# Performance work log

Measured on AMD Instinct MI355X. Metric: run time of the kernel, lower is better.

Reference implementation:

```python
import jax, jax.numpy as jnp
import numpy as np

D_MODEL = 512; D_STATE = 64; D_CONV = 4; EXPAND = 1; HEADDIM = 128; NGROUPS = 2; CHUNK = 256
D_INNER = EXPAND * (D_MODEL // 2)          # 256
NHEADS = D_INNER // HEADDIM                 # 2
CONV_DIM = D_INNER + 2 * NGROUPS * D_STATE  # 512
D_IN_PROJ = CONV_DIM + NHEADS               # 514

def silu(x):
    return x * jax.nn.sigmoid(x)

def conv1x1(x, w, b):
    # x: (b,c,h,w), w: (o,c)
    return jnp.einsum('bchw,oc->bohw', x, w) + b[None, :, None, None]

def dwconv3x3(x, w, b):
    # depthwise 3x3, SAME padding; w: (c,1,3,3)
    c = x.shape[1]
    y = jax.lax.conv_general_dilated(x, w, (1, 1), 'SAME', feature_group_count=c,
                                     dimension_numbers=('NCHW', 'OIHW', 'NCHW'))
    return y + b[None, :, None, None]

def causal_dwconv1d(x, w, b):
    # x: (b,L,c); w: (c,k). Torch pads k-1 both sides then slices [:L] -> causal left pad.
    k = w.shape[1]
    xp = jnp.pad(x, ((0, 0), (k - 1, 0), (0, 0))).transpose(0, 2, 1)  # (b,c,L+k-1)
    y = jax.lax.conv_general_dilated(xp, w[:, None, :], (1,), 'VALID',
                                     feature_group_count=w.shape[0],
                                     dimension_numbers=('NCH', 'OIH', 'NCH'))
    return y.transpose(0, 2, 1) + b

def axis_attn(x, qw, qb, fw, fb, axis):
    # DualAxisAggAttn single-axis step
    qkv = conv1x1(x, qw, qb)
    c = x.shape[1]
    q, k, v = qkv[:, :1], qkv[:, 1:1 + c], qkv[:, 1 + c:]
    dim = -1 if axis == 'W' else -2
    scores = jax.nn.softmax(q, axis=dim)
    ctx = jnp.sum(k * scores, axis=dim, keepdims=True)
    out = x + jax.nn.sigmoid(v) * ctx
    return conv1x1(out, fw, fb)

def segsum(x):
    # x: (...,T) -> (...,T,T) lower-triangular segment sums, -inf above diagonal
    T = x.shape[-1]
    cs = jnp.cumsum(x, -1)
    d = cs[..., :, None] - cs[..., None, :]
    mask = jnp.tril(jnp.ones((T, T), bool))
    return jnp.where(mask, d, -jnp.inf)

def ssd(X, A, B, C, chunk):
    # Mamba2 SSD chunked scan. X: (b,l,h,p) = x*dt; A: (b,l,h) = dt*A_head; B,C: (b,l,h,n)
    b, l, h, p = X.shape; n = B.shape[-1]; c = l // chunk
    X = X.reshape(b, c, chunk, h, p)
    B = B.reshape(b, c, chunk, h, n)
    C = C.reshape(b, c, chunk, h, n)
    A = A.reshape(b, c, chunk, h).transpose(0, 3, 1, 2)  # (b,h,c,L)
    Acs = jnp.cumsum(A, -1)
    L = jnp.exp(segsum(A))  # (b,h,c,L,L) intra-chunk decay
    Yd = jnp.einsum('bclhn,bcshn,bhcls,bcshp->bclhp', C, B, L, X)
    dec = jnp.exp(Acs[..., -1:] - Acs)
    st = jnp.einsum('bclhn,bhcl,bclhp->bchpn', B, dec, X)  # chunk end-states
    st = jnp.concatenate([jnp.zeros_like(st[:, :1]), st], 1)
    dchunk = jnp.exp(segsum(jnp.pad(Acs[..., -1], ((0, 0), (0, 0), (1, 0)))))
    st = jnp.einsum('bhzc,bchpn->bzhpn', dchunk, st)[:, :-1]  # states entering each chunk
    Yo = jnp.einsum('bclhn,bchpn,bhcl->bclhp', C, st, jnp.exp(Acs))
    return (Yd + Yo).reshape(b, l, h, p)

def setup_inputs() -> dict:
    key = jax.random.key(0)
    ks = jax.random.split(key, 12)
    s = 0.02
    p = {}
    p['u'] = jax.random.normal(ks[0], (8, D_MODEL, 64, 64), jnp.float32)
    p['sc_w1'] = jax.random.normal(ks[1], (D_MODEL, D_MODEL)) * s
    p['sc_b1'] = jnp.zeros((D_MODEL,))
    p['sc_wdw'] = jax.random.normal(ks[2], (D_MODEL, 1, 3, 3)) * s
    p['sc_bdw'] = jnp.zeros((D_MODEL,))
    p['sc_w2'] = jax.random.normal(ks[3], (D_INNER, D_MODEL)) * s
    p['sc_b2'] = jnp.zeros((D_INNER,))
    p['mc_w'] = jax.random.normal(ks[4], (D_INNER, D_MODEL)) * s
    p['mc_b'] = jnp.zeros((D_INNER,))
    p['qkvW_w'] = jax.random.normal(ks[5], (1 + 2 * D_INNER, D_INNER)) * s
    p['qkvW_b'] = jnp.zeros((1 + 2 * D_INNER,))
    p['qkvH_w'] = jax.random.normal(ks[6], (1 + 2 * D_INNER, D_INNER)) * s
    p['qkvH_b'] = jnp.zeros((1 + 2 * D_INNER,))
    p['fuseW_w'] = jax.random.normal(ks[7], (D_INNER, D_INNER)) * s
    p['fuseW_b'] = jnp.zeros((D_INNER,))
    p['fuseH_w'] = jax.random.normal(ks[8], (D_INNER, D_INNER)) * s
    p['fuseH_b'] = jnp.zeros((D_INNER,))
    p['in_proj_w'] = jax.random.normal(ks[9], (D_IN_PROJ, D_INNER)) * s
    p['conv1d_w'] = jax.random.normal(ks[10], (CONV_DIM, D_CONV)) * s
    p['conv1d_b'] = jnp.zeros((CONV_DIM,))
    dt = np.exp(np.linspace(np.log(1e-3), np.log(0.1), NHEADS))
    p['dt_bias'] = jnp.asarray(dt + np.log(-np.expm1(-dt)), jnp.float32)
    p['A_log'] = jnp.asarray(np.log(np.linspace(1.0, 16.0, NHEADS)), jnp.float32)
    p['D'] = jnp.ones((NHEADS,))
    p['norm_w'] = jnp.ones((D_INNER,))
    p['outp_w'] = jax.random.normal(ks[11], (D_MODEL, 2 * D_INNER)) * s
    p['outp_b'] = jnp.zeros((D_MODEL,))
    return p

def reference(u, sc_w1, sc_b1, sc_wdw, sc_bdw, sc_w2, sc_b2, mc_w, mc_b,
              qkvW_w, qkvW_b, qkvH_w, qkvH_b, fuseW_w, fuseW_b, fuseH_w, fuseH_b,
              in_proj_w, conv1d_w, conv1d_b, dt_bias, A_log, D, norm_w, outp_w, outp_b):
    b, _, H, W = u.shape
    # short_conv branch (light_ConvBlock: 1x1 -> dw3x3 -> 1x1, all SiLU; BN folded into bias)
    z = silu(conv1x1(u, sc_w1, sc_b1))
    z = silu(dwconv3x3(z, sc_wdw, sc_bdw))
    z = silu(conv1x1(z, sc_w2, sc_b2))
    # main branch
    x = silu(conv1x1(u, mc_w, mc_b))
    x = axis_attn(x, qkvW_w, qkvW_b, fuseW_w, fuseW_b, 'W')
    x = axis_attn(x, qkvH_w, qkvH_b, fuseH_w, fuseH_b, 'H')
    seqlen = H * W
    u2 = x.transpose(0, 2, 3, 1).reshape(b, seqlen, D_INNER)  # b (h w) c
    xbcdt = u2 @ in_proj_w.T  # (b,l,d_in_proj)
    xBC = xbcdt[..., :CONV_DIM]
    dt = jax.nn.softplus(xbcdt[..., CONV_DIM:] + dt_bias)  # (b,l,h)
    A = -jnp.exp(A_log)  # (h,)
    xBC = silu(causal_dwconv1d(xBC, conv1d_w, conv1d_b))
    xs = xBC[..., :D_INNER]
    Bs = xBC[..., D_INNER:D_INNER + NGROUPS * D_STATE].reshape(b, seqlen, NGROUPS, D_STATE)
    Cs = xBC[..., D_INNER + NGROUPS * D_STATE:].reshape(b, seqlen, NGROUPS, D_STATE)
    Xh = xs.reshape(b, seqlen, NHEADS, HEADDIM)
    rep = NHEADS // NGROUPS
    Bh = jnp.repeat(Bs, rep, axis=2)
    Ch = jnp.repeat(Cs, rep, axis=2)
    y = ssd(Xh * dt[..., None], dt * A[None, None, :], Bh, Ch, CHUNK)
    y = y + Xh * D[None, None, :, None]  # D skip connection
    y = y.reshape(b, seqlen, D_INNER)
    # RMSNormGated with z=None -> plain RMSNorm
    y = y * jax.lax.rsqrt(jnp.mean(y * y, -1, keepdims=True) + 1e-5) * norm_w
    y = y.reshape(b, H, W, D_INNER).transpose(0, 3, 1, 2)
    y = jnp.concatenate([z, y], axis=1)
    return conv1x1(y, outp_w, outp_b)
```

## Files before the change

kernel.cpp:

```cpp
#include <hip/hip_runtime.h>
#include <hip/hip_bf16.h>
#include <cstddef>
#include <cstdint>

#define PTOT 32768
#define HWSZ 4096

typedef __attribute__((ext_vector_type(8))) short bf16x8;
typedef __attribute__((ext_vector_type(4))) short s16x4;
typedef __attribute__((ext_vector_type(4))) float f32x4;

__device__ __forceinline__ float sigf(float x){ return 1.f/(1.f+__expf(-x)); }
__device__ __forceinline__ float siluf(float x){ return x*sigf(x); }
__device__ __forceinline__ short f2b(float x){
  __hip_bfloat16 h = __float2bfloat16(x);
  return *reinterpret_cast<short*>(&h);
}
__device__ __forceinline__ float b2f(short s){
  unsigned u = ((unsigned)(unsigned short)s) << 16;
  return __uint_as_float(u);
}

__device__ __forceinline__ void gload16(const void* g, void* l){
  __builtin_amdgcn_global_load_lds(
      (const __attribute__((address_space(1))) unsigned int*)g,
      (__attribute__((address_space(3))) unsigned int*)l, 16, 0, 0);
}

__global__ __launch_bounds__(256) void k_cvtw(
    const float* __restrict__ s0, const float* __restrict__ s1, const float* __restrict__ s2,
    const float* __restrict__ s3, const float* __restrict__ s4,
    short* __restrict__ dst){
  int idx = blockIdx.x*256 + threadIdx.x;
  const float* s; int off;
  if      (idx <  262144){ s=s0; off=idx; }
  else if (idx <  393216){ s=s1; off=idx- 262144; }
  else if (idx <  524288){ s=s2; off=idx- 393216; }
  else if (idx <  655616){ s=s3; off=idx- 524288; }
  else if (idx <  917760){ s=s4; off=idx- 655616; }
  else return;
  dst[idx] = f2b(s[off]);
}

__global__ __launch_bounds__(256) void k_wcomp(
    const float* __restrict__ qkvHw, const float* __restrict__ fuWw,
    const float* __restrict__ fuWb,  const float* __restrict__ qkvHb,
    const float* __restrict__ inpw,  const float* __restrict__ fuHw,
    const float* __restrict__ fuHb,
    const float* __restrict__ scb1,  const float* __restrict__ mcb,
    short* __restrict__ wcomb, float* __restrict__ bcomb,
    short* __restrict__ wi2,   float* __restrict__ bi2,
    float* __restrict__ bzx)
{
  int blk = blockIdx.x;
  int tid = threadIdx.x;
  __shared__ float as[256];
  __shared__ float red[256];
  if (blk < 513){
    int i = blk;
    int r = (i==512) ? 0 : (i+1);
    as[tid]  = qkvHw[(size_t)r*256 + tid];
    red[tid] = as[tid] * fuWb[tid];
    __syncthreads();
    for (int off=128; off; off>>=1){ if (tid<off) red[tid]+=red[tid+off]; __syncthreads(); }
    float acc = 0.f;
    #pragma unroll 8
    for (int k=0;k<256;k++) acc += as[k]*fuWw[(size_t)k*256 + tid];
    wcomb[(size_t)(256+i)*256 + tid] = f2b(acc);
    if (tid==0) bcomb[256+i] = red[0] + qkvHb[r];
  } else if (blk < 769){
    int j = blk - 513;
    wcomb[(size_t)j*256 + tid] = f2b(fuWw[(size_t)j*256 + tid]);
    if (tid==0) bcomb[j] = fuWb[j];
  } else if (blk < 1283){
    int j = blk - 769;
    as[tid]  = inpw[(size_t)j*256 + tid];
    red[tid] = as[tid] * fuHb[tid];
    __syncthreads();
    for (int off=128; off; off>>=1){ if (tid<off) red[tid]+=red[tid+off]; __syncthreads(); }
    float acc = 0.f;
    #pragma unroll 8
    for (int k=0;k<256;k++) acc += as[k]*fuHw[(size_t)k*256 + tid];
    wi2[(size_t)j*256 + tid] = f2b(acc);
    if (tid==0) bi2[j] = red[0];
  } else {
    int j = (blk - 1283)*256 + tid;
    bzx[j] = (j < 512) ? scb1[j] : mcb[j-512];
  }
}

__global__ __launch_bounds__(256) void k_transpose(const float* __restrict__ in, short* __restrict__ out){
  __shared__ float tile[64][33];
  int b = blockIdx.z;
  int c0 = blockIdx.y * 64;
  int s0 = blockIdx.x * 32;
  int tx = threadIdx.x, ty = threadIdx.y;
  const float* ip = in + ((size_t)b*512 + c0)*HWSZ + s0;
  for (int i = ty; i < 64; i += 8) tile[i][tx] = ip[(size_t)i*HWSZ + tx];
  __syncthreads();
  for (int i = ty; i < 32; i += 8){
    unsigned lo = (unsigned)(unsigned short)f2b(tile[2*tx][i]);
    unsigned hi = (unsigned)(unsigned short)f2b(tile[2*tx+1][i]);
    unsigned pk = lo | (hi<<16);
    *reinterpret_cast<unsigned*>(&out[((size_t)((b<<12) + s0 + i))*512 + c0 + 2*tx]) = pk;
  }
}

template<int ACT, int OUT_NCHW>
__global__ __launch_bounds__(256) void k_gemm(
    const short* __restrict__ A0, const short* __restrict__ A1,
    int kSplit, int lda0, int lda1,
    const short* __restrict__ Wt, const float* __restrict__ bias,
    void* __restrict__ Cpv, int N, int K, int ldc, int qkvPerm,
    short* __restrict__ Cp2, int nSplit2, int ldc2)
{
  __shared__ short Alds[3][128*32];
  __shared__ short Wlds[2][128*32];

  int tid = threadIdx.x;
  int lane = tid & 63;
  int wv = tid >> 6;
  int wr = wv >> 1, wc = wv & 1;
  int lr = lane & 15, lh = lane >> 4;
  int bm = blockIdx.x * 128;
  int bn = blockIdx.y * 128;

  int rl = lane >> 2;
  int kg = (lane & 3) << 3;

  int ar[2], wnr[2];
  #pragma unroll
  for (int j=0;j<2;j++){
    int r = wv*32 + j*16 + rl;
    ar[j] = bm + r;
    int n = bn + r; if (n > N-1) n = N-1;
    wnr[j] = qkvPerm ? ((n==512)?0:(n+1)) : n;
  }

  auto stage_a = [&](int buf, int t){
    int k0 = t << 5;
    #pragma unroll
    for (int j=0;j<2;j++){
      const short* asrc;
      if (k0 < kSplit) asrc = A0 + (size_t)ar[j]*lda0 + (k0 + kg);
      else             asrc = A1 + (size_t)ar[j]*lda1 + (k0 - kSplit + kg);
      gload16(asrc, &Alds[buf][(wv*32 + j*16)*32]);
    }
  };
  auto stage_w = [&](int buf, int t){
    int k0 = t << 5;
    #pragma unroll
    for (int j=0;j<2;j++){
      const short* bsrc = Wt + (size_t)wnr[j]*K + (k0 + kg);
      gload16(bsrc, &Wlds[buf][(wv*32 + j*16)*32]);
    }
  };

  f32x4 acc[4][4];
  #pragma unroll
  for (int i=0;i<4;i++)
    #pragma unroll
    for (int j=0;j<4;j++) acc[i][j] = (f32x4){0.f,0.f,0.f,0.f};

  int NT = K >> 5;
  stage_w(0, 0);
  __builtin_amdgcn_sched_barrier(0);
  stage_a(0, 0);
  __builtin_amdgcn_sched_barrier(0);
  stage_a(1, 1);
  for (int t=0; t<NT; t++){
    int ab = t % 3, wb = t & 1;
    if (t+1 < NT) asm volatile("s_waitcnt vmcnt(2)" ::: "memory");
    else          asm volatile("s_waitcnt vmcnt(0)" ::: "memory");
    __builtin_amdgcn_s_barrier();
    __builtin_amdgcn_sched_barrier(0);
    if (t+1 < NT) stage_w(wb^1, t+1);
    __builtin_amdgcn_sched_barrier(0);
    if (t+2 < NT) stage_a((t+2)%3, t+2);
    __builtin_amdgcn_sched_barrier(0);
    bf16x8 af[4], bfr[4];
    #pragma unroll
    for (int mi=0;mi<4;mi++)
      af[mi] = *reinterpret_cast<const bf16x8*>(&Alds[ab][(wr*64 + mi*16 + lr)*32 + lh*8]);
    #pragma unroll
    for (int ni=0;ni<4;ni++)
      bfr[ni] = *reinterpret_cast<const bf16x8*>(&Wlds[wb][(wc*64 + ni*16 + lr)*32 + lh*8]);
    #pragma unroll
    for (int mi=0;mi<4;mi++)
      #pragma unroll
      for (int ni=0;ni<4;ni++)
        acc[mi][ni] = __builtin_amdgcn_mfma_f32_16x16x32_bf16(af[mi], bfr[ni], acc[mi][ni], 0, 0, 0);
  }

  if (!OUT_NCHW){
    short* Cp = (short*)Cpv;
    #pragma unroll
    for (int mi=0;mi<4;mi++){
      int m = bm + wr*64 + mi*16 + lh*4;
      #pragma unroll
      for (int ni=0;ni<4;ni++){
        int n = bn + wc*64 + ni*16 + lr;
        if (n < N){
          int wn = qkvPerm ? ((n==512)?0:(n+1)) : n;
          float bb = bias ? bias[wn] : 0.f;
          #pragma unroll
          for (int r=0;r<4;r++){
            float v = acc[mi][ni][r] + bb;
            if (ACT==1) v = siluf(v);
            short sv = f2b(v);
            if (n < nSplit2) Cp[(size_t)(m+r)*ldc + n] = sv;
            else             Cp2[(size_t)(m+r)*ldc2 + (n - nSplit2)] = sv;
          }
        }
      }
    }
  } else {
    float* Cp = (float*)Cpv;
    float* Sep = ((float*)Alds) + wv*16*68;
    #pragma unroll
    for (int mi=0;mi<4;mi++){
      __syncthreads();
      #pragma unroll
      for (int ni=0;ni<4;ni++){
        int n = bn + wc*64 + ni*16 + lr;
        float bb = (bias && n < N) ? bias[n] : 0.f;
        #pragma unroll
        for (int r=0;r<4;r++){
          float v = acc[mi][ni][r] + bb;
          if (ACT==1) v = siluf(v);
          Sep[(lh*4+r)*68 + ni*16 + lr] = v;
        }
      }
      __syncthreads();
      int m = bm + wr*64 + mi*16 + lr;
      size_t mb = ((size_t)(m>>12)*ldc)*HWSZ + (m & 4095);
      #pragma unroll
      for (int g=0; g<16; g++){
        int nl = g*4 + lh;
        float v = Sep[lr*68 + nl];
        int nn = bn + wc*64 + nl;
        if (nn < N) Cp[mb + (size_t)nn*HWSZ] = v;
      }
    }
  }
}

__global__ __launch_bounds__(256) void k_dwconv3x3(const short* __restrict__ in,
    const float* __restrict__ w, const float* __restrict__ bias, short* __restrict__ out){
  int tid = threadIdx.x;
  int cq = tid & 127;
  int wi = tid >> 7;
  int bw = blockIdx.x;
  int b  = bw >> 5;
  int wc = ((bw & 31) << 1) | wi;
  int h0 = blockIdx.y << 4;
  int c  = cq << 2;

  float arr[36];
  {
    const float* wp = &w[c*9];
    #pragma unroll
    for (int t=0;t<9;t++){
      f32x4 v = *reinterpret_cast<const f32x4*>(wp + t*4);
      arr[t*4+0]=v[0]; arr[t*4+1]=v[1]; arr[t*4+2]=v[2]; arr[t*4+3]=v[3];
    }
  }
  f32x4 bias4 = *reinterpret_cast<const f32x4*>(&bias[c]);

  int pb = b << 12;
  auto ldrow = [&](int r, int dw)->f32x4 {
    int ww = wc + dw;
    if ((unsigned)r >= 64u || (unsigned)ww >= 64u) return (f32x4){0.f,0.f,0.f,0.f};
    s16x4 v = *reinterpret_cast<const s16x4*>(&in[((size_t)(pb + (r<<6) + ww) << 9) + c]);
    return (f32x4){b2f(v[0]), b2f(v[1]), b2f(v[2]), b2f(v[3])};
  };

  f32x4 a00,a01,a02,a10,a11,a12,a20,a21,a22;
  a00=ldrow(h0-1,-1); a01=ldrow(h0-1,0); a02=ldrow(h0-1,1);
  a10=ldrow(h0  ,-1); a11=ldrow(h0  ,0); a12=ldrow(h0  ,1);
  #pragma unroll
  for (int hh=0; hh<16; hh++){
    int h = h0 + hh;
    a20=ldrow(h+1,-1); a21=ldrow(h+1,0); a22=ldrow(h+1,1);
    s16x4 o;
    #pragma unroll
    for (int j=0;j<4;j++){
      float v = bias4[j];
      v = fmaf(a00[j], arr[j*9+0], v);
      v = fmaf(a01[j], arr[j*9+1], v);
      v = fmaf(a02[j], arr[j*9+2], v);
      v = fmaf(a10[j], arr[j*9+3], v);
      v = fmaf(a11[j], arr[j*9+4], v);
      v = fmaf(a12[j], arr[j*9+5], v);
      v = fmaf(a20[j], arr[j*9+6], v);
      v = fmaf(a21[j], arr[j*9+7], v);
      v = fmaf(a22[j], arr[j*9+8], v);
      o[j] = f2b(siluf(v));
    }
    *reinterpret_cast<s16x4*>(&out[((size_t)(pb + (h<<6) + wc) << 9) + c]) = o;
    a00=a10; a01=a11; a02=a12;
    a10=a20; a11=a21; a12=a22;
  }
}

__global__ __launch_bounds__(256) void k_attn(const short* __restrict__ x, int xld,
    const short* __restrict__ qkv, int qld, short* __restrict__ out, int axisH){
  int bl = blockIdx.x;
  int b = bl >> 6, line = bl & 63;
  __shared__ float es[64];
  __shared__ float qs[64];
  int tid = threadIdx.x;
  int pbase = b << 12;
  if (tid < 64){
    int p = axisH ? (pbase | (tid<<6) | line) : (pbase | (line<<6) | tid);
    qs[tid] = b2f(qkv[(size_t)p*qld + 512]);
  }
  __syncthreads();
  float mx = -1e30f;
  for (int t=0;t<64;t++) mx = fmaxf(mx, qs[t]);
  if (tid < 64) es[tid] = __expf(qs[tid]-mx);
  __syncthreads();
  float s = 0.f;
  for (int t=0;t<64;t++) s += es[t];
  float inv = 1.f/s;
  int c = tid;
  float ctx = 0.f;
  for (int t=0;t<64;t++){
    int p = axisH ? (pbase | (t<<6) | line) : (pbase | (line<<6) | t);
    ctx += es[t]*b2f(qkv[(size_t)p*qld + c]);
  }
  ctx *= inv;
  for (int t=0;t<64;t++){
    int p = axisH ? (pbase | (t<<6) | line) : (pbase | (line<<6) | t);
    float vv = b2f(qkv[(size_t)p*qld + 256 + c]);
    float xv = b2f(x[(size_t)p*xld + c]);
    out[(size_t)p*256 + c] = f2b(xv + sigf(vv)*ctx);
  }
}

__global__ __launch_bounds__(256) void k_dt(const short* __restrict__ xbcdt,
    const float* __restrict__ dt_bias, float* __restrict__ dtb){
  int idx = blockIdx.x*256 + threadIdx.x;
  if (idx >= PTOT*2) return;
  int p = idx >> 1, h = idx & 1;
  float xv = b2f(xbcdt[(size_t)p*520 + 512 + h]) + dt_bias[h];
  float sp = (xv > 20.f) ? xv : log1pf(__expf(xv));
  dtb[idx] = sp;
}

__global__ __launch_bounds__(256) void k_conv1d(const short* __restrict__ xbcdt,
    const float* __restrict__ w, const float* __restrict__ bias, short* __restrict__ xBC){
  int tid = threadIdx.x;
  int cq = tid & 127;
  int c  = cq << 2;
  int half = tid >> 7;
  int bs = blockIdx.x;
  int b  = bs >> 7;
  int t0 = ((((bs & 127) << 1) | half) << 4);

  float wk[16];
  {
    const float* wp = &w[c*4];
    #pragma unroll
    for (int t=0;t<4;t++){
      f32x4 v = *reinterpret_cast<const f32x4*>(wp + t*4);
      wk[t*4+0]=v[0]; wk[t*4+1]=v[1]; wk[t*4+2]=v[2]; wk[t*4+3]=v[3];
    }
  }
  f32x4 bias4 = *reinterpret_cast<const f32x4*>(&bias[c]);

  int pb = b << 12;
  auto ld = [&](int t)->f32x4 {
    if (t < 0) return (f32x4){0.f,0.f,0.f,0.f};
    s16x4 v = *reinterpret_cast<const s16x4*>(&xbcdt[(size_t)(pb + t)*520 + c]);
    return (f32x4){b2f(v[0]), b2f(v[1]), b2f(v[2]), b2f(v[3])};
  };

  f32x4 x0,x1,x2,x3;
  x0 = ld(t0-3); x1 = ld(t0-2); x2 = ld(t0-1);
  #pragma unroll
  for (int tt=0; tt<16; tt++){
    int t = t0 + tt;
    x3 = ld(t);
    s16x4 o;
    #pragma unroll
    for (int j=0;j<4;j++){
      float v = bias4[j];
      v = fmaf(x0[j], wk[j*4+0], v);
      v = fmaf(x1[j], wk[j*4+1], v);
      v = fmaf(x2[j], wk[j*4+2], v);
      v = fmaf(x3[j], wk[j*4+3], v);
      o[j] = f2b(siluf(v));
    }
    *reinterpret_cast<s16x4*>(&xBC[((size_t)(pb + t) << 9) + c]) = o;
    x0=x1; x1=x2; x2=x3;
  }
}

__global__ __launch_bounds__(256) void k_ssd_states(
  const short* __restrict__ xBC, const float* __restrict__ dtb, const float* __restrict__ A_log,
  float* __restrict__ states, float* __restrict__ AcsG, float* __restrict__ AtotG)
{
  int ci = blockIdx.x, h = blockIdx.y, b = blockIdx.z;
  int tid = threadIdx.x, lane = tid & 63, wv = tid >> 6;
  int lg = lane >> 4, lr = lane & 15;
  __shared__ float sa[256], sb[256];
  __shared__ short Bt[64*72];
  __shared__ short Xt[128*72];
  int base = (b<<12) | (ci<<8);
  float Ah = -__expf(A_log[h]);
  sa[tid] = dtb[(size_t)(base + tid)*2 + h] * Ah;
  __syncthreads();
  float* src = sa; float* dst = sb;
  for (int off=1; off<256; off<<=1){
    float v = src[tid];
    if (tid >= off) v += src[tid - off];
    dst[tid] = v;
    __syncthreads();
    float* tswap = src; src = dst; dst = tswap;
  }
  float acs = src[tid];
  float atot = src[255];
  AcsG[((size_t)((b*2+h)*16 + ci))*256 + tid] = acs;
  if (tid == 0) AtotG[(b*2+h)*16 + ci] = atot;

  f32x4 acc[8];
  #pragma unroll
  for (int pf=0;pf<8;pf++) acc[pf] = (f32x4){0.f,0.f,0.f,0.f};

  for (int t0=0; t0<256; t0+=64){
    __syncthreads();
    {
      int t = tid >> 2;
      int n0 = (tid & 3) << 4;
      float d = __expf(atot - src[t0 + t]);
      const short* sp = &xBC[(size_t)(base + t0 + t)*512 + 256 + (h<<6) + n0];
      bf16x8 v0 = *reinterpret_cast<const bf16x8*>(sp);
      bf16x8 v1 = *reinterpret_cast<const bf16x8*>(sp+8);
      #pragma unroll
      for (int e=0;e<8;e++) Bt[(n0+e)*72 + t]   = f2b(b2f(v0[e])*d);
      #pragma unroll
      for (int e=0;e<8;e++) Bt[(n0+8+e)*72 + t] = f2b(b2f(v1[e])*d);
    }
    {
      int t = tid >> 2;
      int p0 = (tid & 3) << 5;
      float dtv = dtb[(size_t)(base + t0 + t)*2 + h];
      const short* sp = &xBC[(size_t)(base + t0 + t)*512 + (h<<7) + p0];
      #pragma unroll
      for (int q=0;q<4;q++){
        bf16x8 v = *reinterpret_cast<const bf16x8*>(sp + q*8);
        #pragma unroll
        for (int e=0;e<8;e++) Xt[(p0 + q*8 + e)*72 + t] = f2b(b2f(v[e])*dtv);
      }
    }
    __syncthreads();
    #pragma unroll
    for (int kk=0; kk<2; kk++){
      bf16x8 af = *reinterpret_cast<const bf16x8*>(&Bt[(wv*16 + lr)*72 + kk*32 + lg*8]);
      #pragma unroll
      for (int pf=0;pf<8;pf++){
        bf16x8 xf = *reinterpret_cast<const bf16x8*>(&Xt[(pf*16 + lr)*72 + kk*32 + lg*8]);
        acc[pf] = __builtin_amdgcn_mfma_f32_16x16x32_bf16(af, xf, acc[pf], 0, 0, 0);
      }
    }
  }
  float* stp = states + (((size_t)(b*16+ci)*2 + h) << 13);
  #pragma unroll
  for (int pf=0;pf<8;pf++){
    #pragma unroll
    for (int r=0;r<4;r++)
      stp[(wv*16 + lg*4 + r)*128 + pf*16 + lr] = acc[pf][r];
  }
}

__global__ __launch_bounds__(256) void k_ssd_scan(const float* __restrict__ states,
    const float* __restrict__ AtotG, float* __restrict__ R){
  int bh = blockIdx.x;
  int b = bh >> 1, h = bh & 1;
  int tid = threadIdx.x;
  float r[32];
  #pragma unroll
  for (int j=0;j<32;j++) r[j]=0.f;
  for (int ci=0; ci<16; ci++){
    size_t off = (((size_t)(b*16+ci)*2) + h) << 13;
    #pragma unroll
    for (int j=0;j<32;j++) R[off + tid + (j<<8)] = r[j];
    if (ci < 15){
      float sc = __expf(AtotG[bh*16 + ci]);
      #pragma unroll
      for (int j=0;j<32;j++) r[j] = fmaf(sc, r[j], states[off + tid + (j<<8)]);
    }
  }
}

__global__ __launch_bounds__(256) void k_ssd_y(
  const short* __restrict__ xBC, const float* __restrict__ dtb,
  const float* __restrict__ AcsG, const float* __restrict__ R,
  const float* __restrict__ Dp, float* __restrict__ yraw)
{
  int bx = blockIdx.x;
  int ci = bx >> 2, lt = bx & 3;
  int h = blockIdx.y, b = blockIdx.z;
  int tid = threadIdx.x, lane = tid & 63, w = tid >> 6;
  int lg = lane >> 4, lr = lane & 15;
  int base = (b<<12) | (ci<<8);
  int l0 = lt << 6;

  __shared__ short Cbf[64*72];
  __shared__ short Bbf[64*72];
  __shared__ short Xt [128*76];
  __shared__ short Sbf[64*72];
  __shared__ float acs_l[64], acs_s[64], dt_s[64];

  const float* acsrow = AcsG + ((size_t)((b*2+h)*16 + ci))*256;

  {
    int row = tid >> 2, c0 = (tid & 3) << 4;
    const short* src = &xBC[(size_t)(base + l0 + row)*512 + 384 + (h<<6) + c0];
    *reinterpret_cast<bf16x8*>(&Cbf[row*72 + c0])     = *reinterpret_cast<const bf16x8*>(src);
    *reinterpret_cast<bf16x8*>(&Cbf[row*72 + c0 + 8]) = *reinterpret_cast<const bf16x8*>(src+8);
  }
  if (tid < 64) acs_l[tid] = acsrow[l0 + tid];

  f32x4 yacc[8];
  #pragma unroll
  for (int pf=0;pf<8;pf++) yacc[pf] = (f32x4){0.f,0.f,0.f,0.f};

  for (int s0 = 0; s0 <= l0; s0 += 64){
    __syncthreads();
    {
      int row = tid >> 2, c0 = (tid & 3) << 4;
      const short* src = &xBC[(size_t)(base + s0 + row)*512 + 256 + (h<<6) + c0];
      *reinterpret_cast<bf16x8*>(&Bbf[row*72 + c0])     = *reinterpret_cast<const bf16x8*>(src);
      *reinterpret_cast<bf16x8*>(&Bbf[row*72 + c0 + 8]) = *reinterpret_cast<const bf16x8*>(src+8);
    }
    {
      int s = tid >> 2;
      int p0 = (tid & 3) << 5;
      const short* src = &xBC[(size_t)(base + s0 + s)*512 + (h<<7) + p0];
      #pragma unroll
      for (int q=0;q<4;q++){
        bf16x8 v = *reinterpret_cast<const bf16x8*>(src + q*8);
        #pragma unroll
        for (int e=0;e<8;e++) Xt[(p0 + q*8 + e)*76 + s] = v[e];
      }
    }
    if (tid < 64){
      acs_s[tid] = acsrow[s0 + tid];
      dt_s[tid]  = dtb[(size_t)(base + s0 + tid)*2 + h];
    }
    __syncthreads();

    f32x4 sacc[4];
    #pragma unroll
    for (int f=0;f<4;f++) sacc[f] = (f32x4){0.f,0.f,0.f,0.f};
    bf16x8 ca0 = *reinterpret_cast<const bf16x8*>(&Cbf[(w*16+lr)*72 + lg*8]);
    bf16x8 ca1 = *reinterpret_cast<const bf16x8*>(&Cbf[(w*16+lr)*72 + 32 + lg*8]);
    #pragma unroll
    for (int f=0;f<4;f++){
      bf16x8 bb0 = *reinterpret_cast<const bf16x8*>(&Bbf[(f*16+lr)*72 + lg*8]);
      bf16x8 bb1 = *reinterpret_cast<const bf16x8*>(&Bbf[(f*16+lr)*72 + 32 + lg*8]);
      sacc[f] = __builtin_amdgcn_mfma_f32_16x16x32_bf16(ca0, bb0, sacc[f], 0, 0, 0);
      sacc[f] = __builtin_amdgcn_mfma_f32_16x16x32_bf16(ca1, bb1, sacc[f], 0, 0, 0);
    }
    #pragma unroll
    for (int f=0;f<4;f++){
      #pragma unroll
      for (int r=0;r<4;r++){
        int ll = w*16 + lg*4 + r;
        int ss = f*16 + lr;
        float v = 0.f;
        if (s0 + ss <= l0 + ll)
          v = sacc[f][r] * __expf(acs_l[ll] - acs_s[ss]) * dt_s[ss];
        Sbf[ll*72 + ss] = f2b(v);
      }
    }
    __syncthreads();

    bf16x8 sa0 = *reinterpret_cast<const bf16x8*>(&Sbf[(w*16+lr)*72 + lg*8]);
    bf16x8 sa1 = *reinterpret_cast<const bf16x8*>(&Sbf[(w*16+lr)*72 + 32 + lg*8]);
    #pragma unroll
    for (int pf=0;pf<8;pf++){
      bf16x8 x0 = *reinterpret_cast<const bf16x8*>(&Xt[(pf*16+lr)*76 + lg*8]);
      bf16x8 x1 = *reinterpret_cast<const bf16x8*>(&Xt[(pf*16+lr)*76 + 32 + lg*8]);
      yacc[pf] = __builtin_amdgcn_mfma_f32_16x16x32_bf16(sa0, x0, yacc[pf], 0, 0, 0);
      yacc[pf] = __builtin_amdgcn_mfma_f32_16x16x32_bf16(sa1, x1, yacc[pf], 0, 0, 0);
    }
  }

  __syncthreads();
  {
    size_t roff = (((size_t)(b*16+ci)*2) + h) << 13;
    int n = tid >> 2;
    const float* src = R + roff + (size_t)n*128;
    #pragma unroll
    for (int j=0;j<8;j++){
      int p = ((tid & 3) << 2) + (j << 4);
      float4 f = *reinterpret_cast<const float4*>(&src[p]);
      Xt[(p+0)*76 + n] = f2b(f.x);
      Xt[(p+1)*76 + n] = f2b(f.y);
      Xt[(p+2)*76 + n] = f2b(f.z);
      Xt[(p+3)*76 + n] = f2b(f.w);
    }
  }
  __syncthreads();
  f32x4 racc[8];
  #pragma unroll
  for (int pf=0;pf<8;pf++) racc[pf] = (f32x4){0.f,0.f,0.f,0.f};
  {
    bf16x8 ca0 = *reinterpret_cast<const bf16x8*>(&Cbf[(w*16+lr)*72 + lg*8]);
    bf16x8 ca1 = *reinterpret_cast<const bf16x8*>(&Cbf[(w*16+lr)*72 + 32 + lg*8]);
    #pragma unroll
    for (int pf=0;pf<8;pf++){
      bf16x8 x0 = *reinterpret_cast<const bf16x8*>(&Xt[(pf*16+lr)*76 + lg*8]);
      bf16x8 x1 = *reinterpret_cast<const bf16x8*>(&Xt[(pf*16+lr)*76 + 32 + lg*8]);
      racc[pf] = __builtin_amdgcn_mfma_f32_16x16x32_bf16(ca0, x0, racc[pf], 0, 0, 0);
      racc[pf] = __builtin_amdgcn_mfma_f32_16x16x32_bf16(ca1, x1, racc[pf], 0, 0, 0);
    }
  }

  float Dh = Dp[h];
  float el[4];
  #pragma unroll
  for (int r=0;r<4;r++) el[r] = __expf(acs_l[w*16 + lg*4 + r]);
  #pragma unroll
  for (int pf=0;pf<8;pf++){
    #pragma unroll
    for (int r=0;r<4;r++){
      int ll = w*16 + lg*4 + r;
      int p = pf*16 + lr;
      size_t pix = (size_t)(base + l0 + ll);
      float xraw = b2f(xBC[pix*512 + (h<<7) + p]);
      yraw[pix*256 + (h<<7) + p] = yacc[pf][r] + el[r]*racc[pf][r] + Dh*xraw;
    }
  }
}

__global__ __launch_bounds__(256) void k_rmsnorm(const float* __restrict__ yraw,
    const float* __restrict__ nw, short* __restrict__ ynorm){
  int tid = threadIdx.x, lane = tid & 63, wv = tid >> 6;
  int p = blockIdx.x*4 + wv;
  f32x4 v = *reinterpret_cast<const f32x4*>(&yraw[(size_t)p*256 + lane*4]);
  float sq = v[0]*v[0] + v[1]*v[1] + v[2]*v[2] + v[3]*v[3];
  #pragma unroll
  for (int off=32; off; off>>=1) sq += __shfl_down(sq, off);
  sq = __shfl(sq, 0);
  float scale = rsqrtf(sq*(1.f/256.f) + 1e-5f);
  f32x4 w4 = *reinterpret_cast<const f32x4*>(&nw[lane*4]);
  s16x4 o;
  #pragma unroll
  for (int j=0;j<4;j++) o[j] = f2b(v[j]*scale*w4[j]);
  *reinterpret_cast<s16x4*>(&ynorm[(size_t)p*256 + lane*4]) = o;
}

extern "C" void kernel_launch(void* const* d_in, const int* in_sizes, int n_in,
                              void* d_out, int out_size, void* d_ws, size_t ws_size,
                              hipStream_t stream)
{
  (void)in_sizes; (void)n_in; (void)out_size; (void)ws_size;
  const float* u        = (const float*)d_in[0];
  const float* sc_w1    = (const float*)d_in[1];
  const float* sc_b1    = (const float*)d_in[2];
  const float* sc_wdw   = (const float*)d_in[3];
  const float* sc_bdw   = (const float*)d_in[4];
  const float* sc_w2    = (const float*)d_in[5];
  const float* sc_b2    = (const float*)d_in[6];
  const float* mc_w     = (const float*)d_in[7];
  const float* mc_b     = (const float*)d_in[8];
  const float* qkvW_w   = (const float*)d_in[9];
  const float* qkvW_b   = (const float*)d_in[10];
  const float* qkvH_w   = (const float*)d_in[11];
  const float* qkvH_b   = (const float*)d_in[12];
  const float* fuseW_w  = (const float*)d_in[13];
  const float* fuseW_b  = (const float*)d_in[14];
  const float* fuseH_w  = (const float*)d_in[15];
  const float* fuseH_b  = (const float*)d_in[16];
  const float* in_proj_w= (const float*)d_in[17];
  const float* conv1d_w = (const float*)d_in[18];
  const float* conv1d_b = (const float*)d_in[19];
  const float* dt_bias  = (const float*)d_in[20];
  const float* A_log    = (const float*)d_in[21];
  const float* Dp       = (const float*)d_in[22];
  const float* norm_w   = (const float*)d_in[23];
  const float* outp_w   = (const float*)d_in[24];
  const float* outp_b   = (const float*)d_in[25];

  char* wsb = (char*)d_ws;
  size_t off = 0;
  auto alloc = [&](size_t bytes){ void* p = wsb + off; off = (off + bytes + 255) & ~(size_t)255; return p; };
  short* wbf   = (short*)alloc((size_t)1246208*2);
  float* bcomb = (float*)alloc(769*4);
  float* bi2   = (float*)alloc(514*4);
  float* bzx   = (float*)alloc(768*4);
  short* slotB = (short*)alloc((size_t)PTOT*776*2);
  short* slotC = (short*)alloc((size_t)PTOT*512*2);
  short* slotZ = (short*)alloc((size_t)PTOT*256*2);
  short* slotE = (short*)alloc((size_t)PTOT*256*2);
  float* slotF = (float*)alloc((size_t)PTOT*256*4);
  float* slotS = (float*)alloc((size_t)4460000*4);

  float* dtb     = slotS;
  float* AcsG    = slotS + 65536;
  float* AtotG   = slotS + 131072;
  float* statesB = slotS + 131328;
  float* Rb      = slotS + 131328 + 2097152;
  short* ynorm   = slotE;
  short* xwh     = (short*)slotF;

  short* w_zx   = wbf + 0;
  short* w_sc2  = wbf + 393216;
  short* w_qkvW = wbf + 524288;
  short* w_outp = wbf + 655616;
  short* wcomb  = wbf + 917760;
  short* wi2    = wbf + 1114624;

  short* u_pm = (short*)d_out;
  float* out  = (float*)d_out;

  const int BIG = 1<<30;

  k_cvtw<<<3585, 256, 0, stream>>>(sc_w1, mc_w, sc_w2, qkvW_w, outp_w, wbf);
  k_wcomp<<<1286, 256, 0, stream>>>(qkvH_w, fuseW_w, fuseW_b, qkvH_b, in_proj_w, fuseH_w, fuseH_b,
                                    sc_b1, mc_b, wcomb, bcomb, wi2, bi2, bzx);
  k_transpose<<<dim3(128,8,8), dim3(32,8), 0, stream>>>(u, u_pm);

  k_gemm<1,0><<<dim3(256,6), 256, 0, stream>>>(u_pm, u_pm, BIG, 512, 512, w_zx, bzx,
                                               slotB, 768, 512, 512, 0, slotE, 512, 256);
  k_dwconv3x3<<<dim3(256,4), 256, 0, stream>>>(slotB, sc_wdw, sc_bdw, slotC);
  k_gemm<1,0><<<dim3(256,2), 256, 0, stream>>>(slotC, slotC, BIG, 512, 512, w_sc2, sc_b2,
                                               slotZ, 256, 512, 256, 0, nullptr, BIG, 0);

  k_gemm<0,0><<<dim3(256,5), 256, 0, stream>>>(slotE, slotE, BIG, 256, 256, w_qkvW, qkvW_b,
                                               slotB, 513, 256, 520, 1, nullptr, BIG, 0);
  k_attn<<<512, 256, 0, stream>>>(slotE, 256, slotB, 520, xwh, 0);
  k_gemm<0,0><<<dim3(256,7), 256, 0, stream>>>(xwh, xwh, BIG, 256, 256, wcomb, bcomb,
                                               slotB, 769, 256, 776, 0, nullptr, BIG, 0);
  k_attn<<<512, 256, 0, stream>>>(slotB, 776, slotB + 256, 776, xwh, 1);
  k_gemm<0,0><<<dim3(256,5), 256, 0, stream>>>(xwh, xwh, BIG, 256, 256, wi2, bi2,
                                               slotB, 514, 256, 520, 0, nullptr, BIG, 0);
  k_dt<<<256, 256, 0, stream>>>(slotB, dt_bias, dtb);
  k_conv1d<<<1024, 256, 0, stream>>>(slotB, conv1d_w, conv1d_b, slotC);

  k_ssd_states<<<dim3(16,2,8), 256, 0, stream>>>(slotC, dtb, A_log, statesB, AcsG, AtotG);
  k_ssd_scan<<<16, 256, 0, stream>>>(statesB, AtotG, Rb);
  k_ssd_y<<<dim3(64,2,8), 256, 0, stream>>>(slotC, dtb, AcsG, Rb, Dp, slotF);

  k_rmsnorm<<<8192, 256, 0, stream>>>(slotF, norm_w, ynorm);

  k_gemm<0,1><<<dim3(256,4), 256, 0, stream>>>(slotZ, ynorm, 256, 256, 256, w_outp, outp_b,
                                               out, 512, 512, 512, 0, nullptr, BIG, 0);
}
```

Measured before the change: 436.2 us.

## Split axis attention into ctx/apply kernels and fuse RMSNorm into SSD output

The axis-attention kernel is split into a context reduction kernel, which uses vectorized partial sums across 8 token groups, and a separate fully parallel elementwise apply kernel with 16-byte loads. The earlier version ran serial 64-step loops per thread with scalar strided loads. The SSD output kernel now handles both heads per block and applies RMSNorm in registers using cross-lane shuffles. This removes the fp32 yraw round trip and the separate rmsnorm launch, but halves the SSD grid parallelism and serializes the two heads within a block. ctxb aliases dtb in slotS; that is safe because dtb is computed later.

```diff
diff --git a/kernel.cpp b/kernel.cpp
--- a/kernel.cpp
+++ b/kernel.cpp
@@ -303,39 +303,63 @@
   }
 }
 
-__global__ __launch_bounds__(256) void k_attn(const short* __restrict__ x, int xld,
-    const short* __restrict__ qkv, int qld, short* __restrict__ out, int axisH){
+__global__ __launch_bounds__(256) void k_attn_ctx(const short* __restrict__ qkv, int qld,
+    float* __restrict__ ctx, int axisH){
   int bl = blockIdx.x;
   int b = bl >> 6, line = bl & 63;
-  __shared__ float es[64];
-  __shared__ float qs[64];
   int tid = threadIdx.x;
   int pbase = b << 12;
-  if (tid < 64){
-    int p = axisH ? (pbase | (tid<<6) | line) : (pbase | (line<<6) | tid);
-    qs[tid] = b2f(qkv[(size_t)p*qld + 512]);
-  }
+  __shared__ float qs[64], es[64];
+  __shared__ float part[8][260];
+  auto pos = [&](int t)->int { return axisH ? (pbase | (t<<6) | line) : (pbase | (line<<6) | t); };
+  if (tid < 64) qs[tid] = b2f(qkv[(size_t)pos(tid)*qld + 512]);
   __syncthreads();
   float mx = -1e30f;
   for (int t=0;t<64;t++) mx = fmaxf(mx, qs[t]);
   if (tid < 64) es[tid] = __expf(qs[tid]-mx);
   __syncthreads();
+  int tg = tid >> 5;
+  int cg = tid & 31;
+  float pacc[8];
+  #pragma unroll
+  for (int j=0;j<8;j++) pacc[j]=0.f;
+  #pragma unroll
+  for (int tt=0; tt<8; tt++){
+    int t = tg*8 + tt;
+    bf16x8 kv = *reinterpret_cast<const bf16x8*>(&qkv[(size_t)pos(t)*qld + cg*8]);
+    float e = es[t];
+    #pragma unroll
+    for (int j=0;j<8;j++) pacc[j] = fmaf(e, b2f(kv[j]), pacc[j]);
+  }
+  #pragma unroll
+  for (int j=0;j<8;j++) part[tg][cg*8+j] = pacc[j];
+  __syncthreads();
   float s = 0.f;
   for (int t=0;t<64;t++) s += es[t];
   float inv = 1.f/s;
   int c = tid;
-  float ctx = 0.f;
-  for (int t=0;t<64;t++){
-    int p = axisH ? (pbase | (t<<6) | line) : (pbase | (line<<6) | t);
-    ctx += es[t]*b2f(qkv[(size_t)p*qld + c]);
-  }
-  ctx *= inv;
-  for (int t=0;t<64;t++){
-    int p = axisH ? (pbase | (t<<6) | line) : (pbase | (line<<6) | t);
-    float vv = b2f(qkv[(size_t)p*qld + 256 + c]);
-    float xv = b2f(x[(size_t)p*xld + c]);
-    out[(size_t)p*256 + c] = f2b(xv + sigf(vv)*ctx);
-  }
+  float v = 0.f;
+  #pragma unroll
+  for (int g=0; g<8; g++) v += part[g][c];
+  ctx[(size_t)bl*256 + c] = v*inv;
+}
+
+__global__ __launch_bounds__(256) void k_attn_apply(const short* __restrict__ x, int xld,
+    const short* __restrict__ qkv, int qld, const float* __restrict__ ctx,
+    short* __restrict__ out, int axisH){
+  int idx = blockIdx.x*256 + threadIdx.x;
+  int p = idx >> 5;
+  int c0 = (idx & 31) << 3;
+  int line = axisH ? (p & 63) : ((p >> 6) & 63);
+  int bl = (p >> 12)*64 + line;
+  bf16x8 vv = *reinterpret_cast<const bf16x8*>(&qkv[(size_t)p*qld + 256 + c0]);
+  bf16x8 xv = *reinterpret_cast<const bf16x8*>(&x[(size_t)p*xld + c0]);
+  const float* cp = &ctx[(size_t)bl*256 + c0];
+  bf16x8 o;
+  #pragma unroll
+  for (int j=0;j<8;j++)
+    o[j] = f2b(b2f(xv[j]) + sigf(b2f(vv[j]))*cp[j]);
+  *reinterpret_cast<bf16x8*>(&out[(size_t)p*256 + c0]) = o;
 }
 
 __global__ __launch_bounds__(256) void k_dt(const short* __restrict__ xbcdt,
@@ -494,14 +518,14 @@
   }
 }
 
-__global__ __launch_bounds__(256) void k_ssd_y(
+__global__ __launch_bounds__(256) void k_ssd_y_norm(
   const short* __restrict__ xBC, const float* __restrict__ dtb,
   const float* __restrict__ AcsG, const float* __restrict__ R,
-  const float* __restrict__ Dp, float* __restrict__ yraw)
+  const float* __restrict__ Dp, const float* __restrict__ nw, short* __restrict__ ynorm)
 {
   int bx = blockIdx.x;
   int ci = bx >> 2, lt = bx & 3;
-  int h = blockIdx.y, b = blockIdx.z;
+  int b = blockIdx.y;
   int tid = threadIdx.x, lane = tid & 63, w = tid >> 6;
   int lg = lane >> 4, lr = lane & 15;
   int base = (b<<12) | (ci<<8);
@@ -513,145 +537,163 @@
   __shared__ short Sbf[64*72];
   __shared__ float acs_l[64], acs_s[64], dt_s[64];
 
-  const float* acsrow = AcsG + ((size_t)((b*2+h)*16 + ci))*256;
-
-  {
-    int row = tid >> 2, c0 = (tid & 3) << 4;
-    const short* src = &xBC[(size_t)(base + l0 + row)*512 + 384 + (h<<6) + c0];
-    *reinterpret_cast<bf16x8*>(&Cbf[row*72 + c0])     = *reinterpret_cast<const bf16x8*>(src);
-    *reinterpret_cast<bf16x8*>(&Cbf[row*72 + c0 + 8]) = *reinterpret_cast<const bf16x8*>(src+8);
-  }
-  if (tid < 64) acs_l[tid] = acsrow[l0 + tid];
-
-  f32x4 yacc[8];
-  #pragma unroll
-  for (int pf=0;pf<8;pf++) yacc[pf] = (f32x4){0.f,0.f,0.f,0.f};
-
-  for (int s0 = 0; s0 <= l0; s0 += 64){
+  auto body = [&](int h, f32x4* yv){
+    __syncthreads();
+    const float* acsrow = AcsG + ((size_t)((b*2+h)*16 + ci))*256;
+    {
+      int row = tid >> 2, c0 = (tid & 3) << 4;
+      const short* src = &xBC[(size_t)(base + l0 + row)*512 + 384 + (h<<6) + c0];
+      *reinterpret_cast<bf16x8*>(&Cbf[row*72 + c0])     = *reinterpret_cast<const bf16x8*>(src);
+      *reinterpret_cast<bf16x8*>(&Cbf[row*72 + c0 + 8]) = *reinterpret_cast<const bf16x8*>(src+8);
+    }
+    if (tid < 64) acs_l[tid] = acsrow[l0 + tid];
+
+    f32x4 yacc[8];
+    #pragma unroll
+    for (int pf=0;pf<8;pf++) yacc[pf] = (f32x4){0.f,0.f,0.f,0.f};
+
+    for (int s0 = 0; s0 <= l0; s0 += 64){
+      __syncthreads();
+      {
+        int row = tid >> 2, c0 = (tid & 3) << 4;
+        const short* src = &xBC[(size_t)(base + s0 + row)*512 + 256 + (h<<6) + c0];
+        *reinterpret_cast<bf16x8*>(&Bbf[row*72 + c0])     = *reinterpret_cast<const bf16x8*>(src);
+        *reinterpret_cast<bf16x8*>(&Bbf[row*72 + c0 + 8]) = *reinterpret_cast<const bf16x8*>(src+8);
+      }
+      {
+        int s = tid >> 2;
+        int p0 = (tid & 3) << 5;
+        const short* src = &xBC[(size_t)(base + s0 + s)*512 + (h<<7) + p0];
+        #pragma unroll
+        for (int q=0;q<4;q++){
+          bf16x8 v = *reinterpret_cast<const bf16x8*>(src + q*8);
+          #pragma unroll
+          for (int e=0;e<8;e++) Xt[(p0 + q*8 + e)*76 + s] = v[e];
+        }
+      }
+      if (tid < 64){
+        acs_s[tid] = acsrow[s0 + tid];
+        dt_s[tid]  = dtb[(size_t)(base + s0 + tid)*2 + h];
+      }
+      __syncthreads();
+
+      f32x4 sacc[4];
+      #pragma unroll
+      for (int f=0;f<4;f++) sacc[f] = (f32x4){0.f,0.f,0.f,0.f};
+      bf16x8 ca0 = *reinterpret_cast<const bf16x8*>(&Cbf[(w*16+lr)*72 + lg*8]);
+      bf16x8 ca1 = *reinterpret_cast<const bf16x8*>(&Cbf[(w*16+lr)*72 + 32 + lg*8]);
+      #pragma unroll
+      for (int f=0;f<4;f++){
+        bf16x8 bb0 = *reinterpret_cast<const bf16x8*>(&Bbf[(f*16+lr)*72 + lg*8]);
+        bf16x8 bb1 = *reinterpret_cast<const bf16x8*>(&Bbf[(f*16+lr)*72 + 32 + lg*8]);
+        sacc[f] = __builtin_amdgcn_mfma_f32_16x16x32_bf16(ca0, bb0, sacc[f], 0, 0, 0);
+        sacc[f] = __builtin_amdgcn_mfma_f32_16x16x32_bf16(ca1, bb1, sacc[f], 0, 0, 0);
+      }
+      #pragma unroll
+      for (int f=0;f<4;f++){
+        #pragma unroll
+        for (int r=0;r<4;r++){
+          int ll = w*16 + lg*4 + r;
+          int ss = f*16 + lr;
+          float v = 0.f;
+          if (s0 + ss <= l0 + ll)
+            v = sacc[f][r] * __expf(acs_l[ll] - acs_s[ss]) * dt_s[ss];
+          Sbf[ll*72 + ss] = f2b(v);
+        }
+      }
+      __syncthreads();
+
+      bf16x8 sa0 = *reinterpret_cast<const bf16x8*>(&Sbf[(w*16+lr)*72 + lg*8]);
+      bf16x8 sa1 = *reinterpret_cast<const bf16x8*>(&Sbf[(w*16+lr)*72 + 32 + lg*8]);
+      #pragma unroll
+      for (int pf=0;pf<8;pf++){
+        bf16x8 x0 = *reinterpret_cast<const bf16x8*>(&Xt[(pf*16+lr)*76 + lg*8]);
+        bf16x8 x1 = *reinterpret_cast<const bf16x8*>(&Xt[(pf*16+lr)*76 + 32 + lg*8]);
+        yacc[pf] = __builtin_amdgcn_mfma_f32_16x16x32_bf16(sa0, x0, yacc[pf], 0, 0, 0);
+        yacc[pf] = __builtin_amdgcn_mfma_f32_16x16x32_bf16(sa1, x1, yacc[pf], 0, 0, 0);
+      }
+    }
+
     __syncthreads();
     {
-      int row = tid >> 2, c0 = (tid & 3) << 4;
-      const short* src = &xBC[(size_t)(base + s0 + row)*512 + 256 + (h<<6) + c0];
-      *reinterpret_cast<bf16x8*>(&Bbf[row*72 + c0])     = *reinterpret_cast<const bf16x8*>(src);
-      *reinterpret_cast<bf16x8*>(&Bbf[row*72 + c0 + 8]) = *reinterpret_cast<const bf16x8*>(src+8);
-    }
+      size_t roff = (((size_t)(b*16+ci)*2) + h) << 13;
+      int n = tid >> 2;
+      const float* src = R + roff + (size_t)n*128;
+      #pragma unroll
+      for (int j=0;j<8;j++){
+        int p = ((tid & 3) << 2) + (j << 4);
+        float4 f = *reinterpret_cast<const float4*>(&src[p]);
+        Xt[(p+0)*76 + n] = f2b(f.x);
+        Xt[(p+1)*76 + n] = f2b(f.y);
+        Xt[(p+2)*76 + n] = f2b(f.z);
+        Xt[(p+3)*76 + n] = f2b(f.w);
+      }
+    }
+    __syncthreads();
+    f32x4 racc[8];
+    #pragma unroll
+    for (int pf=0;pf<8;pf++) racc[pf] = (f32x4){0.f,0.f,0.f,0.f};
     {
-      int s = tid >> 2;
-      int p0 = (tid & 3) << 5;
-      const short* src = &xBC[(size_t)(base + s0 + s)*512 + (h<<7) + p0];
-      #pragma unroll
-      for (int q=0;q<4;q++){
-        bf16x8 v = *reinterpret_cast<const bf16x8*>(src + q*8);
-        #pragma unroll
-        for (int e=0;e<8;e++) Xt[(p0 + q*8 + e)*76 + s] = v[e];
-      }
-    }
-    if (tid < 64){
-      acs_s[tid] = acsrow[s0 + tid];
-      dt_s[tid]  = dtb[(size_t)(base + s0 + tid)*2 + h];
-    }
-    __syncthreads();
-
-    f32x4 sacc[4];
-    #pragma unroll
-    for (int f=0;f<4;f++) sacc[f] = (f32x4){0.f,0.f,0.f,0.f};
-    bf16x8 ca0 = *reinterpret_cast<const bf16x8*>(&Cbf[(w*16+lr)*72 + lg*8]);
-    bf16x8 ca1 = *reinterpret_cast<const bf16x8*>(&Cbf[(w*16+lr)*72 + 32 + lg*8]);
-    #pragma unroll
-    for (int f=0;f<4;f++){
-      bf16x8 bb0 = *reinterpret_cast<const bf16x8*>(&Bbf[(f*16+lr)*72 + lg*8]);
-      bf16x8 bb1 = *reinterpret_cast<const bf16x8*>(&Bbf[(f*16+lr)*72 + 32 + lg*8]);
-      sacc[f] = __builtin_amdgcn_mfma_f32_16x16x32_bf16(ca0, bb0, sacc[f], 0, 0, 0);
-      sacc[f] = __builtin_amdgcn_mfma_f32_16x16x32_bf16(ca1, bb1, sacc[f], 0, 0, 0);
-    }
-    #pragma unroll
-    for (int f=0;f<4;f++){
+      bf16x8 ca0 = *reinterpret_cast<const bf16x8*>(&Cbf[(w*16+lr)*72 + lg*8]);
+      bf16x8 ca1 = *reinterpret_cast<const bf16x8*>(&Cbf[(w*16+lr)*72 + 32 + lg*8]);
+      #pragma unroll
+      for (int pf=0;pf<8;pf++){
+        bf16x8 x0 = *reinterpret_cast<const bf16x8*>(&Xt[(pf*16+lr)*76 + lg*8]);
+        bf16x8 x1 = *reinterpret_cast<const bf16x8*>(&Xt[(pf*16+lr)*76 + 32 + lg*8]);
+        racc[pf] = __builtin_amdgcn_mfma_f32_16x16x32_bf16(ca0, x0, racc[pf], 0, 0, 0);
+        racc[pf] = __builtin_amdgcn_mfma_f32_16x16x32_bf16(ca1, x1, racc[pf], 0, 0, 0);
+      }
+    }
+    float Dh = Dp[h];
+    float el[4];
+    #pragma unroll
+    for (int r=0;r<4;r++) el[r] = __expf(acs_l[w*16 + lg*4 + r]);
+    #pragma unroll
+    for (int pf=0;pf<8;pf++){
+      f32x4 o;
       #pragma unroll
       for (int r=0;r<4;r++){
         int ll = w*16 + lg*4 + r;
-        int ss = f*16 + lr;
-        float v = 0.f;
-        if (s0 + ss <= l0 + ll)
-          v = sacc[f][r] * __expf(acs_l[ll] - acs_s[ss]) * dt_s[ss];
-        Sbf[ll*72 + ss] = f2b(v);
-      }
-    }
-    __syncthreads();
-
-    bf16x8 sa0 = *reinterpret_cast<const bf16x8*>(&Sbf[(w*16+lr)*72 + lg*8]);
-    bf16x8 sa1 = *reinterpret_cast<const bf16x8*>(&Sbf[(w*16+lr)*72 + 32 + lg*8]);
-    #pragma unroll
-    for (int pf=0;pf<8;pf++){
-      bf16x8 x0 = *reinterpret_cast<const bf16x8*>(&Xt[(pf*16+lr)*76 + lg*8]);
-      bf16x8 x1 = *reinterpret_cast<const bf16x8*>(&Xt[(pf*16+lr)*76 + 32 + lg*8]);
-      yacc[pf] = __builtin_amdgcn_mfma_f32_16x16x32_bf16(sa0, x0, yacc[pf], 0, 0, 0);
-      yacc[pf] = __builtin_amdgcn_mfma_f32_16x16x32_bf16(sa1, x1, yacc[pf], 0, 0, 0);
-    }
-  }
-
-  __syncthreads();
-  {
-    size_t roff = (((size_t)(b*16+ci)*2) + h) << 13;
-    int n = tid >> 2;
-    const float* src = R + roff + (size_t)n*128;
-    #pragma unroll
-    for (int j=0;j<8;j++){
-      int p = ((tid & 3) << 2) + (j << 4);
-      float4 f = *reinterpret_cast<const float4*>(&src[p]);
-      Xt[(p+0)*76 + n] = f2b(f.x);
-      Xt[(p+1)*76 + n] = f2b(f.y);
-      Xt[(p+2)*76 + n] = f2b(f.z);
-      Xt[(p+3)*76 + n] = f2b(f.w);
-    }
-  }
-  __syncthreads();
-  f32x4 racc[8];
-  #pragma unroll
-  for (int pf=0;pf<8;pf++) racc[pf] = (f32x4){0.f,0.f,0.f,0.f};
-  {
-    bf16x8 ca0 = *reinterpret_cast<const bf16x8*>(&Cbf[(w*16+lr)*72 + lg*8]);
-    bf16x8 ca1 = *reinterpret_cast<const bf16x8*>(&Cbf[(w*16+lr)*72 + 32 + lg*8]);
-    #pragma unroll
-    for (int pf=0;pf<8;pf++){
-      bf16x8 x0 = *reinterpret_cast<const bf16x8*>(&Xt[(pf*16+lr)*76 + lg*8]);
-      bf16x8 x1 = *reinterpret_cast<const bf16x8*>(&Xt[(pf*16+lr)*76 + 32 + lg*8]);
-      racc[pf] = __builtin_amdgcn_mfma_f32_16x16x32_bf16(ca0, x0, racc[pf], 0, 0, 0);
-      racc[pf] = __builtin_amdgcn_mfma_f32_16x16x32_bf16(ca1, x1, racc[pf], 0, 0, 0);
-    }
-  }
-
-  float Dh = Dp[h];
-  float el[4];
-  #pragma unroll
-  for (int r=0;r<4;r++) el[r] = __expf(acs_l[w*16 + lg*4 + r]);
+        int p = pf*16 + lr;
+        size_t pix = (size_t)(base + l0 + ll);
+        float xraw = b2f(xBC[pix*512 + (h<<7) + p]);
+        o[r] = yacc[pf][r] + el[r]*racc[pf][r] + Dh*xraw;
+      }
+      yv[pf] = o;
+    }
+  };
+
+  f32x4 y0[8], y1[8];
+  body(0, y0);
+  body(1, y1);
+
+  f32x4 ss = (f32x4){0.f,0.f,0.f,0.f};
   #pragma unroll
   for (int pf=0;pf<8;pf++){
     #pragma unroll
+    for (int r=0;r<4;r++)
+      ss[r] += y0[pf][r]*y0[pf][r] + y1[pf][r]*y1[pf][r];
+  }
+  #pragma unroll
+  for (int m=1; m<16; m<<=1){
+    #pragma unroll
+    for (int r=0;r<4;r++) ss[r] += __shfl_xor(ss[r], m);
+  }
+  f32x4 scale;
+  #pragma unroll
+  for (int r=0;r<4;r++) scale[r] = rsqrtf(ss[r]*(1.f/256.f) + 1e-5f);
+
+  #pragma unroll
+  for (int pf=0;pf<8;pf++){
+    float nw0 = nw[pf*16 + lr];
+    float nw1 = nw[128 + pf*16 + lr];
+    #pragma unroll
     for (int r=0;r<4;r++){
-      int ll = w*16 + lg*4 + r;
-      int p = pf*16 + lr;
-      size_t pix = (size_t)(base + l0 + ll);
-      float xraw = b2f(xBC[pix*512 + (h<<7) + p]);
-      yraw[pix*256 + (h<<7) + p] = yacc[pf][r] + el[r]*racc[pf][r] + Dh*xraw;
-    }
-  }
-}
-
-__global__ __launch_bounds__(256) void k_rmsnorm(const float* __restrict__ yraw,
-    const float* __restrict__ nw, short* __restrict__ ynorm){
-  int tid = threadIdx.x, lane = tid & 63, wv = tid >> 6;
-  int p = blockIdx.x*4 + wv;
-  f32x4 v = *reinterpret_cast<const f32x4*>(&yraw[(size_t)p*256 + lane*4]);
-  float sq = v[0]*v[0] + v[1]*v[1] + v[2]*v[2] + v[3]*v[3];
-  #pragma unroll
-  for (int off=32; off; off>>=1) sq += __shfl_down(sq, off);
-  sq = __shfl(sq, 0);
-  float scale = rsqrtf(sq*(1.f/256.f) + 1e-5f);
-  f32x4 w4 = *reinterpret_cast<const f32x4*>(&nw[lane*4]);
-  s16x4 o;
-  #pragma unroll
-  for (int j=0;j<4;j++) o[j] = f2b(v[j]*scale*w4[j]);
-  *reinterpret_cast<s16x4*>(&ynorm[(size_t)p*256 + lane*4]) = o;
+      size_t pix = (size_t)(base + l0 + w*16 + lg*4 + r);
+      ynorm[pix*256 + pf*16 + lr]        = f2b(y0[pf][r]*scale[r]*nw0);
+      ynorm[pix*256 + 128 + pf*16 + lr]  = f2b(y1[pf][r]*scale[r]*nw1);
+    }
+  }
 }
 
 extern "C" void kernel_launch(void* const* d_in, const int* in_sizes, int n_in,
@@ -697,7 +739,7 @@
   short* slotC = (short*)alloc((size_t)PTOT*512*2);
   short* slotZ = (short*)alloc((size_t)PTOT*256*2);
   short* slotE = (short*)alloc((size_t)PTOT*256*2);
-  float* slotF = (float*)alloc((size_t)PTOT*256*4);
+  short* slotF = (short*)alloc((size_t)PTOT*256*2);
   float* slotS = (float*)alloc((size_t)4460000*4);
 
   float* dtb     = slotS;
@@ -705,8 +747,9 @@
   float* AtotG   = slotS + 131072;
   float* statesB = slotS + 131328;
   float* Rb      = slotS + 131328 + 2097152;
+  float* ctxb    = slotS;
   short* ynorm   = slotE;
-  short* xwh     = (short*)slotF;
+  short* xwh     = slotF;
 
   short* w_zx   = wbf + 0;
   short* w_sc2  = wbf + 393216;
@@ -733,10 +776,12 @@
 
   k_gemm<0,0><<<dim3(256,5), 256, 0, stream>>>(slotE, slotE, BIG, 256, 256, w_qkvW, qkvW_b,
                                                slotB, 513, 256, 520, 1, nullptr, BIG, 0);
-  k_attn<<<512, 256, 0, stream>>>(slotE, 256, slotB, 520, xwh, 0);
+  k_attn_ctx<<<512, 256, 0, stream>>>(slotB, 520, ctxb, 0);
+  k_attn_apply<<<4096, 256, 0, stream>>>(slotE, 256, slotB, 520, ctxb, xwh, 0);
   k_gemm<0,0><<<dim3(256,7), 256, 0, stream>>>(xwh, xwh, BIG, 256, 256, wcomb, bcomb,
                                                slotB, 769, 256, 776, 0, nullptr, BIG, 0);
-  k_attn<<<512, 256, 0, stream>>>(slotB, 776, slotB + 256, 776, xwh, 1);
+  k_attn_ctx<<<512, 256, 0, stream>>>(slotB + 256, 776, ctxb, 1);
+  k_attn_apply<<<4096, 256, 0, stream>>>(slotB, 776, slotB + 256, 776, ctxb, xwh, 1);
   k_gemm<0,0><<<dim3(256,5), 256, 0, stream>>>(xwh, xwh, BIG, 256, 256, wi2, bi2,
                                                slotB, 514, 256, 520, 0, nullptr, BIG, 0);
   k_dt<<<256, 256, 0, stream>>>(slotB, dt_bias, dtb);
@@ -744,9 +789,7 @@
 
   k_ssd_states<<<dim3(16,2,8), 256, 0, stream>>>(slotC, dtb, A_log, statesB, AcsG, AtotG);
   k_ssd_scan<<<16, 256, 0, stream>>>(statesB, AtotG, Rb);
-  k_ssd_y<<<dim3(64,2,8), 256, 0, stream>>>(slotC, dtb, AcsG, Rb, Dp, slotF);
-
-  k_rmsnorm<<<8192, 256, 0, stream>>>(slotF, norm_w, ynorm);
+  k_ssd_y_norm<<<dim3(64,8), 256, 0, stream>>>(slotC, dtb, AcsG, Rb, Dp, norm_w, ynorm);
 
   k_gemm<0,1><<<dim3(256,4), 256, 0, stream>>>(slotZ, ynorm, 256, 256, 256, w_outp, outp_b,
                                                out, 512, 512, 512, 0, nullptr, BIG, 0);
```

Result: faster. 409.1 us (-6.2%).
